# Kernel optimization log

Measured on AMD Instinct MI355X. Metric: run time of the kernel, lower is better.

## Reference

```python
import jax, jax.numpy as jnp
import numpy as np

B, S, H, E = 4, 4096, 2048, 8
TOP_K = 2

def setup_inputs() -> dict:
    key = jax.random.key(0)
    k0, k1, k2, k3, k4 = jax.random.split(key, 5)
    Hm = H // 2
    return {
        "hidden_states": jax.random.normal(k0, (B, S, H), dtype=jnp.float32),
        "W1": jax.random.normal(k1, (H, Hm), dtype=jnp.float32) * (1.0 / np.sqrt(H)),
        "b1": jnp.zeros((Hm,), dtype=jnp.float32),
        "W2": jax.random.normal(k2, (Hm, E), dtype=jnp.float32) * (1.0 / np.sqrt(Hm)),
        "b2": jnp.zeros((E,), dtype=jnp.float32),
    }

def reference(hidden_states, W1, b1, W2, b2):
    # Router MLP: Linear(H -> H//2) -> ReLU -> Dropout(eval: identity) -> Linear(H//2 -> E)
    h = jax.nn.relu(jnp.einsum("bsh,hm->bsm", hidden_states, W1) + b1)
    router_logits = jnp.einsum("bsm,me->bse", h, W2) + b2  # [B, S, E]
    probs = jax.nn.softmax(router_logits, axis=-1)
    expert_weights, expert_indices = jax.lax.top_k(probs, TOP_K)  # [B, S, 2]
    return (router_logits, expert_weights, expert_indices)
```

## Files before the change

kernel.cpp:

```cpp
#include <hip/hip_runtime.h>
#include <hip/hip_bf16.h>


#define HDIM 2048
#define HM 1024
#define NROWS 16384
#define NE 8
#define KSTEPS 64

typedef _Float16 f16;
typedef f16 f16x8 __attribute__((ext_vector_type(8)));
typedef __fp16 h16x2 __attribute__((ext_vector_type(2)));
typedef float f32x4 __attribute__((ext_vector_type(4)));

union frag8 {
  f16x8 v;
  h16x2 p[4];
};

__device__ __forceinline__ void gload16(const void* g, void* l) {
  __builtin_amdgcn_global_load_lds(
      (const __attribute__((address_space(1))) void*)g,
      (__attribute__((address_space(3))) void*)l, 16, 0, 0);
}

__global__ __launch_bounds__(256) void prep_w1(const float* __restrict__ W1,
                                               f16* __restrict__ W1s) {
  const int nb = blockIdx.x & 3;
  const int ktidx = blockIdx.x >> 2;
  const int r = threadIdx.x;
  const int n = nb * 256 + r;
  const int kt = ktidx * 32;
  f16 hi[32], lo[32];
#pragma unroll
  for (int kk = 0; kk < 32; ++kk) {
    float x = W1[(size_t)(kt + kk) * HM + n];
    f16 h = (f16)x;
    hi[kk] = h;
    lo[kk] = (f16)(x - (float)h);
  }
  f16* dst = W1s + (size_t)(nb * 64 + ktidx) * 16384 + r * 64;
#pragma unroll
  for (int sp = 0; sp < 8; ++sp) {
    int s = sp ^ (r & 7);
    f16x8 v;
#pragma unroll
    for (int j = 0; j < 8; ++j)
      v[j] = (s < 4) ? hi[8 * s + j] : lo[8 * (s - 4) + j];
    *(f16x8*)(dst + sp * 8) = v;
  }
}

__global__ __launch_bounds__(512, 2) void router_mfma(
    const float* __restrict__ X, const f16* __restrict__ W1s,
    const float* __restrict__ b1, const float* __restrict__ W2,
    float* __restrict__ pl) {
  const int bid = blockIdx.x;
  const int wg = (bid & 7) * 32 + (bid >> 3);
  const int rb = wg >> 2;
  const int nb = wg & 3;

  const int t = threadIdx.x;
  const int lane = t & 63;
  const int wave = t >> 6;
  const int wm = wave >> 2;
  const int wn = wave & 3;
  const int lane15 = lane & 15;
  const int lgrp = lane >> 4;

  extern __shared__ char smem[];

  const int srow = t >> 1;
  const int shalf = t & 1;
  const float* Xr = X + (size_t)(rb * 256 + srow) * HDIM + shalf * 16;
  const int sm = srow & 7;
  const int woff_h0 = srow * 128 + (((2 * shalf) ^ sm) << 4);
  const int woff_h1 = srow * 128 + (((2 * shalf + 1) ^ sm) << 4);
  const int woff_l0 = srow * 128 + (((4 + 2 * shalf) ^ sm) << 4);
  const int woff_l1 = srow * 128 + (((5 + 2 * shalf) ^ sm) << 4);

  const char* W1sB = (const char*)W1s + (size_t)nb * 64 * 32768;
  const int t16 = t * 16;

#define GLB(KT, BUF)                                                      \
  {                                                                       \
    char* bB_ = smem + (BUF) * 65536 + 32768;                             \
    _Pragma("unroll")                                                     \
    for (int i_ = 0; i_ < 4; ++i_)                                        \
      gload16(W1sB + (((size_t)(KT)) << 15) + i_ * 8192 + t16,            \
              bB_ + i_ * 8192 + t16);                                     \
  }

#define SPLITWR(BUF, x0, x1, x2, x3)                                      \
  {                                                                       \
    char* bA_ = smem + (BUF) * 65536;                                     \
    frag8 hi0_, hi1_, lo0_, lo1_;                                         \
    hi0_.p[0] = __builtin_amdgcn_cvt_pkrtz(x0.x, x0.y);                   \
    hi0_.p[1] = __builtin_amdgcn_cvt_pkrtz(x0.z, x0.w);                   \
    hi0_.p[2] = __builtin_amdgcn_cvt_pkrtz(x1.x, x1.y);                   \
    hi0_.p[3] = __builtin_amdgcn_cvt_pkrtz(x1.z, x1.w);                   \
    hi1_.p[0] = __builtin_amdgcn_cvt_pkrtz(x2.x, x2.y);                   \
    hi1_.p[1] = __builtin_amdgcn_cvt_pkrtz(x2.z, x2.w);                   \
    hi1_.p[2] = __builtin_amdgcn_cvt_pkrtz(x3.x, x3.y);                   \
    hi1_.p[3] = __builtin_amdgcn_cvt_pkrtz(x3.z, x3.w);                   \
    lo0_.p[0] = __builtin_amdgcn_cvt_pkrtz(x0.x - (float)hi0_.p[0][0],    \
                                           x0.y - (float)hi0_.p[0][1]);   \
    lo0_.p[1] = __builtin_amdgcn_cvt_pkrtz(x0.z - (float)hi0_.p[1][0],    \
                                           x0.w - (float)hi0_.p[1][1]);   \
    lo0_.p[2] = __builtin_amdgcn_cvt_pkrtz(x1.x - (float)hi0_.p[2][0],    \
                                           x1.y - (float)hi0_.p[2][1]);   \
    lo0_.p[3] = __builtin_amdgcn_cvt_pkrtz(x1.z - (float)hi0_.p[3][0],    \
                                           x1.w - (float)hi0_.p[3][1]);   \
    lo1_.p[0] = __builtin_amdgcn_cvt_pkrtz(x2.x - (float)hi1_.p[0][0],    \
                                           x2.y - (float)hi1_.p[0][1]);   \
    lo1_.p[1] = __builtin_amdgcn_cvt_pkrtz(x2.z - (float)hi1_.p[1][0],    \
                                           x2.w - (float)hi1_.p[1][1]);   \
    lo1_.p[2] = __builtin_amdgcn_cvt_pkrtz(x3.x - (float)hi1_.p[2][0],    \
                                           x3.y - (float)hi1_.p[2][1]);   \
    lo1_.p[3] = __builtin_amdgcn_cvt_pkrtz(x3.z - (float)hi1_.p[3][0],    \
                                           x3.w - (float)hi1_.p[3][1]);   \
    *(f16x8*)(bA_ + woff_h0) = hi0_.v;                                    \
    *(f16x8*)(bA_ + woff_h1) = hi1_.v;                                    \
    *(f16x8*)(bA_ + woff_l0) = lo0_.v;                                    \
    *(f16x8*)(bA_ + woff_l1) = lo1_.v;                                    \
  }

  f32x4 acc[8][4];
#pragma unroll
  for (int i = 0; i < 8; ++i)
#pragma unroll
    for (int j = 0; j < 4; ++j) acc[i][j] = (f32x4){0.f, 0.f, 0.f, 0.f};

  {
    GLB(0, 0);
    GLB(1, 1);
    float4 a0 = *(const float4*)(Xr + 0);
    float4 a1 = *(const float4*)(Xr + 4);
    float4 a2 = *(const float4*)(Xr + 8);
    float4 a3 = *(const float4*)(Xr + 12);
    float4 c0 = *(const float4*)(Xr + 32);
    float4 c1 = *(const float4*)(Xr + 36);
    float4 c2 = *(const float4*)(Xr + 40);
    float4 c3 = *(const float4*)(Xr + 44);
    asm volatile("s_waitcnt vmcnt(0)" ::: "memory");
    SPLITWR(0, a0, a1, a2, a3);
    SPLITWR(1, c0, c1, c2, c3);
    asm volatile("s_waitcnt lgkmcnt(0)" ::: "memory");
  }
  __builtin_amdgcn_s_barrier();

  const int arow_base = wm * 128 + lane15;
  const int offAh = ((lgrp ^ (lane15 & 7)) << 4);
  const int offAl = (((4 + lgrp) ^ (lane15 & 7)) << 4);

  int cur = 0;
#pragma unroll 1
  for (int kti = 0; kti < KSTEPS; ++kti) {
    const char* ldsA = smem + cur * 65536;
    const f16* ldsB = (const f16*)(ldsA + 32768);
    const bool stage2 = (kti + 2 < KSTEPS);

    float4 x0, x1, x2, x3;
    if (stage2) {
      const float* xs = Xr + (kti + 2) * 32;
      x0 = *(const float4*)(xs + 0);
      x1 = *(const float4*)(xs + 4);
      x2 = *(const float4*)(xs + 8);
      x3 = *(const float4*)(xs + 12);
    }

    frag8 bh[4], bl[4];
#pragma unroll
    for (int ni = 0; ni < 4; ++ni) {
      int c = wn * 64 + ni * 16 + lane15;
      bh[ni].v = *(const f16x8*)&ldsB[c * 64 + ((lgrp ^ (c & 7)) << 3)];
      bl[ni].v = *(const f16x8*)&ldsB[c * 64 + (((4 + lgrp) ^ (c & 7)) << 3)];
    }

    frag8 ah, al, nah, nal;
    {
      const char* rowp = ldsA + arow_base * 128;
      ah.v = *(const f16x8*)(rowp + offAh);
      al.v = *(const f16x8*)(rowp + offAl);
    }
#pragma unroll
    for (int mi = 0; mi < 8; ++mi) {
      if (mi < 7) {
        const char* rowp = ldsA + (arow_base + (mi + 1) * 16) * 128;
        nah.v = *(const f16x8*)(rowp + offAh);
        nal.v = *(const f16x8*)(rowp + offAl);
      }
      __builtin_amdgcn_s_setprio(1);
#pragma unroll
      for (int ni = 0; ni < 4; ++ni) {
        acc[mi][ni] = __builtin_amdgcn_mfma_f32_16x16x32_f16(
            ah.v, bh[ni].v, acc[mi][ni], 0, 0, 0);
        acc[mi][ni] = __builtin_amdgcn_mfma_f32_16x16x32_f16(
            ah.v, bl[ni].v, acc[mi][ni], 0, 0, 0);
        acc[mi][ni] = __builtin_amdgcn_mfma_f32_16x16x32_f16(
            al.v, bh[ni].v, acc[mi][ni], 0, 0, 0);
      }
      __builtin_amdgcn_s_setprio(0);
      ah = nah;
      al = nal;
    }

    if (kti == KSTEPS - 1) break;
    __builtin_amdgcn_sched_barrier(0);
    __builtin_amdgcn_s_barrier();
    if (stage2) {
      GLB(kti + 2, cur);
      asm volatile("s_waitcnt vmcnt(4)" ::: "memory");
      SPLITWR(cur, x0, x1, x2, x3);
      asm volatile("s_waitcnt lgkmcnt(0)" ::: "memory");
    } else {
      asm volatile("s_waitcnt vmcnt(0)" ::: "memory");
    }
    __builtin_amdgcn_s_barrier();
    cur ^= 1;
  }

  __syncthreads();
  float* red = (float*)smem;

  float bvals[4];
  float w2r[4][NE];
#pragma unroll
  for (int ni = 0; ni < 4; ++ni) {
    int c = nb * 256 + wn * 64 + ni * 16 + lane15;
    bvals[ni] = b1[c];
    const float* src = W2 + (size_t)c * NE;
#pragma unroll
    for (int e = 0; e < NE; ++e) w2r[ni][e] = src[e];
  }

#pragma unroll
  for (int mi = 0; mi < 8; ++mi) {
    float plr[4][NE];
#pragma unroll
    for (int j = 0; j < 4; ++j)
#pragma unroll
      for (int e = 0; e < NE; ++e) plr[j][e] = 0.f;
#pragma unroll
    for (int ni = 0; ni < 4; ++ni) {
#pragma unroll
      for (int j = 0; j < 4; ++j) {
        float h = acc[mi][ni][j] + bvals[ni];
        h = fmaxf(h, 0.f);
#pragma unroll
        for (int e = 0; e < NE; ++e) plr[j][e] = fmaf(h, w2r[ni][e], plr[j][e]);
      }
    }
#pragma unroll
    for (int m = 1; m < 16; m <<= 1)
#pragma unroll
      for (int j = 0; j < 4; ++j)
#pragma unroll
        for (int e = 0; e < NE; ++e)
          plr[j][e] += __shfl_xor(plr[j][e], m, 64);
    if (lane15 == 0) {
#pragma unroll
      for (int j = 0; j < 4; ++j) {
        int rr = wm * 128 + mi * 16 + lgrp * 4 + j;
#pragma unroll
        for (int e = 0; e < NE; ++e)
          red[(size_t)wn * 2048 + rr * NE + e] = plr[j][e];
      }
    }
  }
  __syncthreads();
  for (int i = t; i < 256 * NE; i += 512) {
    int r = i >> 3, e = i & 7;
    int row = rb * 256 + r;
    float s = red[i] + red[2048 + i] + red[4096 + i] + red[6144 + i];
    pl[((size_t)nb * NROWS + row) * NE + e] = s;
  }
}

__global__ __launch_bounds__(256) void router_finalize(
    const float* __restrict__ pl, const float* __restrict__ b2,
    float* __restrict__ out) {
  int row = blockIdx.x * 256 + threadIdx.x;
  if (row >= NROWS) return;
  float l[NE];
#pragma unroll
  for (int e = 0; e < NE; ++e) l[e] = b2[e];
  for (int nb = 0; nb < 4; ++nb) {
    const float* src = pl + ((size_t)nb * NROWS + row) * NE;
#pragma unroll
    for (int e = 0; e < NE; ++e) l[e] += src[e];
  }
#pragma unroll
  for (int e = 0; e < NE; ++e) out[(size_t)row * NE + e] = l[e];

  float m = l[0];
#pragma unroll
  for (int e = 1; e < NE; ++e) m = fmaxf(m, l[e]);
  float p[NE], s = 0.f;
#pragma unroll
  for (int e = 0; e < NE; ++e) {
    p[e] = expf(l[e] - m);
    s += p[e];
  }
  float inv = 1.f / s;

  float v0 = -1.f, v1 = -1.f;
  int i0 = 0, i1 = 0;
#pragma unroll
  for (int e = 0; e < NE; ++e) {
    float pe = p[e];
    if (pe > v0) {
      v1 = v0; i1 = i0;
      v0 = pe; i0 = e;
    } else if (pe > v1) {
      v1 = pe; i1 = e;
    }
  }
  size_t wbase = (size_t)NROWS * NE + (size_t)row * 2;
  out[wbase] = v0 * inv;
  out[wbase + 1] = v1 * inv;
  size_t ibase = (size_t)NROWS * NE + (size_t)NROWS * 2 + (size_t)row * 2;
  out[ibase] = (float)i0;
  out[ibase + 1] = (float)i1;
}

extern "C" void kernel_launch(void* const* d_in, const int* in_sizes, int n_in,
                              void* d_out, int out_size, void* d_ws,
                              size_t ws_size, hipStream_t stream) {
  const float* X = (const float*)d_in[0];
  const float* W1 = (const float*)d_in[1];
  const float* b1 = (const float*)d_in[2];
  const float* W2 = (const float*)d_in[3];
  const float* b2 = (const float*)d_in[4];
  float* out = (float*)d_out;

  float* pl = (float*)d_ws;
  f16* W1s = (f16*)((char*)d_ws + (size_t)4 * 1024 * 1024);

  (void)hipFuncSetAttribute((const void*)router_mfma,
                            hipFuncAttributeMaxDynamicSharedMemorySize, 131072);

  hipLaunchKernelGGL(prep_w1, dim3(256), dim3(256), 0, stream, W1, W1s);
  hipLaunchKernelGGL(router_mfma, dim3(256), dim3(512), 131072, stream, X, W1s,
                     b1, W2, pl);
  hipLaunchKernelGGL(router_finalize, dim3(NROWS / 256), dim3(256), 0, stream,
                     pl, b2, out);
}
```

Baseline: 206.1 us.

## Switch router GEMM from 16x16x32 to 32x32x16 MFMA tiles

Replaces the 16x16x32 f16 MFMA tiling with 32x32x16 MFMAs, each covering half the K step. The swizzled LDS fragment addressing, accumulator layout and fused ReLU/W2 epilogue are reworked to match the 32x32 output layout. The aim is to issue half as many MFMA instructions and use the larger-tile instruction, which may run more efficiently per flop. In exchange, the epilogue reduction now needs five shuffle stages over 32 lanes for 16 row groups, which adds cross-lane shuffle work.

Measured after the change: 255.9 us. 1.24x slower.

```diff
diff --git a/kernel.cpp b/kernel.cpp
--- a/kernel.cpp
+++ b/kernel.cpp
@@ -12,6 +12,7 @@
 typedef f16 f16x8 __attribute__((ext_vector_type(8)));
 typedef __fp16 h16x2 __attribute__((ext_vector_type(2)));
 typedef float f32x4 __attribute__((ext_vector_type(4)));
+typedef float f32x16 __attribute__((ext_vector_type(16)));
 
 union frag8 {
   f16x8 v;
@@ -65,8 +66,8 @@
   const int wave = t >> 6;
   const int wm = wave >> 2;
   const int wn = wave & 3;
-  const int lane15 = lane & 15;
-  const int lgrp = lane >> 4;
+  const int lane31 = lane & 31;
+  const int hi5 = lane >> 5;
 
   extern __shared__ char smem[];
 
@@ -125,11 +126,13 @@
     *(f16x8*)(bA_ + woff_l1) = lo1_.v;                                    \
   }
 
-  f32x4 acc[8][4];
-#pragma unroll
-  for (int i = 0; i < 8; ++i)
-#pragma unroll
-    for (int j = 0; j < 4; ++j) acc[i][j] = (f32x4){0.f, 0.f, 0.f, 0.f};
+  f32x16 acc[4][2];
+#pragma unroll
+  for (int i = 0; i < 4; ++i)
+#pragma unroll
+    for (int j = 0; j < 2; ++j)
+#pragma unroll
+      for (int k = 0; k < 16; ++k) acc[i][j][k] = 0.f;
 
   {
     GLB(0, 0);
@@ -149,15 +152,17 @@
   }
   __builtin_amdgcn_s_barrier();
 
-  const int arow_base = wm * 128 + lane15;
-  const int offAh = ((lgrp ^ (lane15 & 7)) << 4);
-  const int offAl = (((4 + lgrp) ^ (lane15 & 7)) << 4);
+  const int l7 = lane & 7;
+  const int offH[2] = {(((0 + hi5) ^ l7) << 4), (((2 + hi5) ^ l7) << 4)};
+  const int offL[2] = {(((4 + hi5) ^ l7) << 4), (((6 + hi5) ^ l7) << 4)};
+  const int arow0 = (wm * 128 + lane31) * 128;
+  const int bcol0 = (wn * 64 + lane31) * 128;
 
   int cur = 0;
 #pragma unroll 1
   for (int kti = 0; kti < KSTEPS; ++kti) {
     const char* ldsA = smem + cur * 65536;
-    const f16* ldsB = (const f16*)(ldsA + 32768);
+    const char* ldsB = ldsA + 32768;
     const bool stage2 = (kti + 2 < KSTEPS);
 
     float4 x0, x1, x2, x3;
@@ -169,40 +174,58 @@
       x3 = *(const float4*)(xs + 12);
     }
 
-    frag8 bh[4], bl[4];
-#pragma unroll
-    for (int ni = 0; ni < 4; ++ni) {
-      int c = wn * 64 + ni * 16 + lane15;
-      bh[ni].v = *(const f16x8*)&ldsB[c * 64 + ((lgrp ^ (c & 7)) << 3)];
-      bl[ni].v = *(const f16x8*)&ldsB[c * 64 + (((4 + lgrp) ^ (c & 7)) << 3)];
-    }
-
-    frag8 ah, al, nah, nal;
+    frag8 bh[2][2], bl[2][2];
+#pragma unroll
+    for (int ni = 0; ni < 2; ++ni) {
+      const char* cp = ldsB + bcol0 + ni * 32 * 128;
+#pragma unroll
+      for (int ks = 0; ks < 2; ++ks) {
+        bh[ni][ks].v = *(const f16x8*)(cp + offH[ks]);
+        bl[ni][ks].v = *(const f16x8*)(cp + offL[ks]);
+      }
+    }
+
+    frag8 ah[2], al[2], nah[2], nal[2];
     {
-      const char* rowp = ldsA + arow_base * 128;
-      ah.v = *(const f16x8*)(rowp + offAh);
-      al.v = *(const f16x8*)(rowp + offAl);
-    }
-#pragma unroll
-    for (int mi = 0; mi < 8; ++mi) {
-      if (mi < 7) {
-        const char* rowp = ldsA + (arow_base + (mi + 1) * 16) * 128;
-        nah.v = *(const f16x8*)(rowp + offAh);
-        nal.v = *(const f16x8*)(rowp + offAl);
+      const char* rp = ldsA + arow0;
+#pragma unroll
+      for (int ks = 0; ks < 2; ++ks) {
+        ah[ks].v = *(const f16x8*)(rp + offH[ks]);
+        al[ks].v = *(const f16x8*)(rp + offL[ks]);
+      }
+    }
+#pragma unroll
+    for (int mi = 0; mi < 4; ++mi) {
+      if (mi < 3) {
+        const char* rp = ldsA + arow0 + (mi + 1) * 32 * 128;
+#pragma unroll
+        for (int ks = 0; ks < 2; ++ks) {
+          nah[ks].v = *(const f16x8*)(rp + offH[ks]);
+          nal[ks].v = *(const f16x8*)(rp + offL[ks]);
+        }
       }
       __builtin_amdgcn_s_setprio(1);
 #pragma unroll
-      for (int ni = 0; ni < 4; ++ni) {
-        acc[mi][ni] = __builtin_amdgcn_mfma_f32_16x16x32_f16(
-            ah.v, bh[ni].v, acc[mi][ni], 0, 0, 0);
-        acc[mi][ni] = __builtin_amdgcn_mfma_f32_16x16x32_f16(
-            ah.v, bl[ni].v, acc[mi][ni], 0, 0, 0);
-        acc[mi][ni] = __builtin_amdgcn_mfma_f32_16x16x32_f16(
-            al.v, bh[ni].v, acc[mi][ni], 0, 0, 0);
+      for (int ks = 0; ks < 2; ++ks) {
+        acc[mi][0] = __builtin_amdgcn_mfma_f32_32x32x16_f16(
+            ah[ks].v, bh[0][ks].v, acc[mi][0], 0, 0, 0);
+        acc[mi][1] = __builtin_amdgcn_mfma_f32_32x32x16_f16(
+            ah[ks].v, bh[1][ks].v, acc[mi][1], 0, 0, 0);
+        acc[mi][0] = __builtin_amdgcn_mfma_f32_32x32x16_f16(
+            ah[ks].v, bl[0][ks].v, acc[mi][0], 0, 0, 0);
+        acc[mi][1] = __builtin_amdgcn_mfma_f32_32x32x16_f16(
+            ah[ks].v, bl[1][ks].v, acc[mi][1], 0, 0, 0);
+        acc[mi][0] = __builtin_amdgcn_mfma_f32_32x32x16_f16(
+            al[ks].v, bh[0][ks].v, acc[mi][0], 0, 0, 0);
+        acc[mi][1] = __builtin_amdgcn_mfma_f32_32x32x16_f16(
+            al[ks].v, bh[1][ks].v, acc[mi][1], 0, 0, 0);
       }
       __builtin_amdgcn_s_setprio(0);
-      ah = nah;
-      al = nal;
+#pragma unroll
+      for (int ks = 0; ks < 2; ++ks) {
+        ah[ks] = nah[ks];
+        al[ks] = nal[ks];
+      }
     }
 
     if (kti == KSTEPS - 1) break;
@@ -223,11 +246,11 @@
   __syncthreads();
   float* red = (float*)smem;
 
-  float bvals[4];
-  float w2r[4][NE];
-#pragma unroll
-  for (int ni = 0; ni < 4; ++ni) {
-    int c = nb * 256 + wn * 64 + ni * 16 + lane15;
+  float bvals[2];
+  float w2r[2][NE];
+#pragma unroll
+  for (int ni = 0; ni < 2; ++ni) {
+    int c = nb * 256 + wn * 64 + ni * 32 + lane31;
     bvals[ni] = b1[c];
     const float* src = W2 + (size_t)c * NE;
 #pragma unroll
@@ -235,36 +258,40 @@
   }
 
 #pragma unroll
-  for (int mi = 0; mi < 8; ++mi) {
-    float plr[4][NE];
-#pragma unroll
-    for (int j = 0; j < 4; ++j)
-#pragma unroll
-      for (int e = 0; e < NE; ++e) plr[j][e] = 0.f;
-#pragma unroll
-    for (int ni = 0; ni < 4; ++ni) {
-#pragma unroll
-      for (int j = 0; j < 4; ++j) {
-        float h = acc[mi][ni][j] + bvals[ni];
-        h = fmaxf(h, 0.f);
-#pragma unroll
-        for (int e = 0; e < NE; ++e) plr[j][e] = fmaf(h, w2r[ni][e], plr[j][e]);
-      }
-    }
-#pragma unroll
-    for (int m = 1; m < 16; m <<= 1)
+  for (int mi = 0; mi < 4; ++mi) {
+#pragma unroll
+    for (int q = 0; q < 4; ++q) {
+      float plr[4][NE];
 #pragma unroll
       for (int j = 0; j < 4; ++j)
 #pragma unroll
-        for (int e = 0; e < NE; ++e)
-          plr[j][e] += __shfl_xor(plr[j][e], m, 64);
-    if (lane15 == 0) {
-#pragma unroll
-      for (int j = 0; j < 4; ++j) {
-        int rr = wm * 128 + mi * 16 + lgrp * 4 + j;
-#pragma unroll
-        for (int e = 0; e < NE; ++e)
-          red[(size_t)wn * 2048 + rr * NE + e] = plr[j][e];
+        for (int e = 0; e < NE; ++e) plr[j][e] = 0.f;
+#pragma unroll
+      for (int ni = 0; ni < 2; ++ni) {
+#pragma unroll
+        for (int j = 0; j < 4; ++j) {
+          float h = acc[mi][ni][4 * q + j] + bvals[ni];
+          h = fmaxf(h, 0.f);
+#pragma unroll
+          for (int e = 0; e < NE; ++e)
+            plr[j][e] = fmaf(h, w2r[ni][e], plr[j][e]);
+        }
+      }
+#pragma unroll
+      for (int m = 1; m < 32; m <<= 1)
+#pragma unroll
+        for (int j = 0; j < 4; ++j)
+#pragma unroll
+          for (int e = 0; e < NE; ++e)
+            plr[j][e] += __shfl_xor(plr[j][e], m, 64);
+      if (lane31 == 0) {
+#pragma unroll
+        for (int j = 0; j < 4; ++j) {
+          int rr = wm * 128 + mi * 32 + q * 8 + hi5 * 4 + j;
+#pragma unroll
+          for (int e = 0; e < NE; ++e)
+            red[(size_t)wn * 2048 + rr * NE + e] = plr[j][e];
+        }
       }
     }
   }
```

## Use plain fp16 GEMM and recompute near-tie rows exactly in fp32

Applied to the files above, without the earlier changes.

Replaces the split-fp16 (hi/lo) three-MFMA emulation of fp32 with a single fp16 hi×hi product, halving the K-steps and cutting MFMA work by roughly two thirds. Rows whose top logits fall within a small threshold of each other are flagged via an atomic counter and recomputed exactly in fp32 by two new kernels, so top-k selection stays correct. Softmax/top-k is simplified to work on logits directly. The risk is that logits for unflagged rows carry fp16 error, and the fixed capacity on flagged rows may overflow.

Measured after the change: 541.3 us. 163% more time.

```diff
diff --git a/kernel.cpp b/kernel.cpp
--- a/kernel.cpp
+++ b/kernel.cpp
@@ -6,7 +6,8 @@
 #define HM 1024
 #define NROWS 16384
 #define NE 8
-#define KSTEPS 64
+#define KSTEPS 32
+#define TH_FLAG 0.006f
 
 typedef _Float16 f16;
 typedef f16 f16x8 __attribute__((ext_vector_type(8)));
@@ -25,34 +26,29 @@
 }
 
 __global__ __launch_bounds__(256) void prep_w1(const float* __restrict__ W1,
-                                               f16* __restrict__ W1s) {
+                                               f16* __restrict__ W1h) {
   const int nb = blockIdx.x & 3;
-  const int ktidx = blockIdx.x >> 2;
+  const int kt = blockIdx.x >> 2;
   const int r = threadIdx.x;
   const int n = nb * 256 + r;
-  const int kt = ktidx * 32;
-  f16 hi[32], lo[32];
-#pragma unroll
-  for (int kk = 0; kk < 32; ++kk) {
-    float x = W1[(size_t)(kt + kk) * HM + n];
-    f16 h = (f16)x;
-    hi[kk] = h;
-    lo[kk] = (f16)(x - (float)h);
-  }
-  f16* dst = W1s + (size_t)(nb * 64 + ktidx) * 16384 + r * 64;
+  const int k0 = kt * 64;
+  f16 hi[64];
+#pragma unroll
+  for (int kk = 0; kk < 64; ++kk)
+    hi[kk] = (f16)W1[(size_t)(k0 + kk) * HM + n];
+  f16* dst = W1h + (size_t)(nb * 32 + kt) * 16384 + r * 64;
 #pragma unroll
   for (int sp = 0; sp < 8; ++sp) {
     int s = sp ^ (r & 7);
     f16x8 v;
 #pragma unroll
-    for (int j = 0; j < 8; ++j)
-      v[j] = (s < 4) ? hi[8 * s + j] : lo[8 * (s - 4) + j];
+    for (int j = 0; j < 8; ++j) v[j] = hi[8 * s + j];
     *(f16x8*)(dst + sp * 8) = v;
   }
 }
 
 __global__ __launch_bounds__(512, 2) void router_mfma(
-    const float* __restrict__ X, const f16* __restrict__ W1s,
+    const float* __restrict__ X, const f16* __restrict__ W1h,
     const float* __restrict__ b1, const float* __restrict__ W2,
     float* __restrict__ pl) {
   const int bid = blockIdx.x;
@@ -72,14 +68,14 @@
 
   const int srow = t >> 1;
   const int shalf = t & 1;
-  const float* Xr = X + (size_t)(rb * 256 + srow) * HDIM + shalf * 16;
+  const float* Xr = X + (size_t)(rb * 256 + srow) * HDIM + shalf * 32;
   const int sm = srow & 7;
-  const int woff_h0 = srow * 128 + (((2 * shalf) ^ sm) << 4);
-  const int woff_h1 = srow * 128 + (((2 * shalf + 1) ^ sm) << 4);
-  const int woff_l0 = srow * 128 + (((4 + 2 * shalf) ^ sm) << 4);
-  const int woff_l1 = srow * 128 + (((5 + 2 * shalf) ^ sm) << 4);
-
-  const char* W1sB = (const char*)W1s + (size_t)nb * 64 * 32768;
+  int woff[4];
+#pragma unroll
+  for (int i = 0; i < 4; ++i)
+    woff[i] = srow * 128 + (((shalf * 4 + i) ^ sm) << 4);
+
+  const char* W1hB = (const char*)W1h + (size_t)nb * 32 * 32768;
   const int t16 = t * 16;
 
 #define GLB(KT, BUF)                                                      \
@@ -87,42 +83,34 @@
     char* bB_ = smem + (BUF) * 65536 + 32768;                             \
     _Pragma("unroll")                                                     \
     for (int i_ = 0; i_ < 4; ++i_)                                        \
-      gload16(W1sB + (((size_t)(KT)) << 15) + i_ * 8192 + t16,            \
+      gload16(W1hB + (((size_t)(KT)) << 15) + i_ * 8192 + t16,            \
               bB_ + i_ * 8192 + t16);                                     \
   }
 
-#define SPLITWR(BUF, x0, x1, x2, x3)                                      \
+#define HIWR(BUF, X0, X1, X2, X3, X4, X5, X6, X7)                         \
   {                                                                       \
     char* bA_ = smem + (BUF) * 65536;                                     \
-    frag8 hi0_, hi1_, lo0_, lo1_;                                         \
-    hi0_.p[0] = __builtin_amdgcn_cvt_pkrtz(x0.x, x0.y);                   \
-    hi0_.p[1] = __builtin_amdgcn_cvt_pkrtz(x0.z, x0.w);                   \
-    hi0_.p[2] = __builtin_amdgcn_cvt_pkrtz(x1.x, x1.y);                   \
-    hi0_.p[3] = __builtin_amdgcn_cvt_pkrtz(x1.z, x1.w);                   \
-    hi1_.p[0] = __builtin_amdgcn_cvt_pkrtz(x2.x, x2.y);                   \
-    hi1_.p[1] = __builtin_amdgcn_cvt_pkrtz(x2.z, x2.w);                   \
-    hi1_.p[2] = __builtin_amdgcn_cvt_pkrtz(x3.x, x3.y);                   \
-    hi1_.p[3] = __builtin_amdgcn_cvt_pkrtz(x3.z, x3.w);                   \
-    lo0_.p[0] = __builtin_amdgcn_cvt_pkrtz(x0.x - (float)hi0_.p[0][0],    \
-                                           x0.y - (float)hi0_.p[0][1]);   \
-    lo0_.p[1] = __builtin_amdgcn_cvt_pkrtz(x0.z - (float)hi0_.p[1][0],    \
-                                           x0.w - (float)hi0_.p[1][1]);   \
-    lo0_.p[2] = __builtin_amdgcn_cvt_pkrtz(x1.x - (float)hi0_.p[2][0],    \
-                                           x1.y - (float)hi0_.p[2][1]);   \
-    lo0_.p[3] = __builtin_amdgcn_cvt_pkrtz(x1.z - (float)hi0_.p[3][0],    \
-                                           x1.w - (float)hi0_.p[3][1]);   \
-    lo1_.p[0] = __builtin_amdgcn_cvt_pkrtz(x2.x - (float)hi1_.p[0][0],    \
-                                           x2.y - (float)hi1_.p[0][1]);   \
-    lo1_.p[1] = __builtin_amdgcn_cvt_pkrtz(x2.z - (float)hi1_.p[1][0],    \
-                                           x2.w - (float)hi1_.p[1][1]);   \
-    lo1_.p[2] = __builtin_amdgcn_cvt_pkrtz(x3.x - (float)hi1_.p[2][0],    \
-                                           x3.y - (float)hi1_.p[2][1]);   \
-    lo1_.p[3] = __builtin_amdgcn_cvt_pkrtz(x3.z - (float)hi1_.p[3][0],    \
-                                           x3.w - (float)hi1_.p[3][1]);   \
-    *(f16x8*)(bA_ + woff_h0) = hi0_.v;                                    \
-    *(f16x8*)(bA_ + woff_h1) = hi1_.v;                                    \
-    *(f16x8*)(bA_ + woff_l0) = lo0_.v;                                    \
-    *(f16x8*)(bA_ + woff_l1) = lo1_.v;                                    \
+    frag8 v0_, v1_, v2_, v3_;                                             \
+    v0_.p[0] = __builtin_amdgcn_cvt_pkrtz(X0.x, X0.y);                    \
+    v0_.p[1] = __builtin_amdgcn_cvt_pkrtz(X0.z, X0.w);                    \
+    v0_.p[2] = __builtin_amdgcn_cvt_pkrtz(X1.x, X1.y);                    \
+    v0_.p[3] = __builtin_amdgcn_cvt_pkrtz(X1.z, X1.w);                    \
+    v1_.p[0] = __builtin_amdgcn_cvt_pkrtz(X2.x, X2.y);                    \
+    v1_.p[1] = __builtin_amdgcn_cvt_pkrtz(X2.z, X2.w);                    \
+    v1_.p[2] = __builtin_amdgcn_cvt_pkrtz(X3.x, X3.y);                    \
+    v1_.p[3] = __builtin_amdgcn_cvt_pkrtz(X3.z, X3.w);                    \
+    v2_.p[0] = __builtin_amdgcn_cvt_pkrtz(X4.x, X4.y);                    \
+    v2_.p[1] = __builtin_amdgcn_cvt_pkrtz(X4.z, X4.w);                    \
+    v2_.p[2] = __builtin_amdgcn_cvt_pkrtz(X5.x, X5.y);                    \
+    v2_.p[3] = __builtin_amdgcn_cvt_pkrtz(X5.z, X5.w);                    \
+    v3_.p[0] = __builtin_amdgcn_cvt_pkrtz(X6.x, X6.y);                    \
+    v3_.p[1] = __builtin_amdgcn_cvt_pkrtz(X6.z, X6.w);                    \
+    v3_.p[2] = __builtin_amdgcn_cvt_pkrtz(X7.x, X7.y);                    \
+    v3_.p[3] = __builtin_amdgcn_cvt_pkrtz(X7.z, X7.w);                    \
+    *(f16x8*)(bA_ + woff[0]) = v0_.v;                                     \
+    *(f16x8*)(bA_ + woff[1]) = v1_.v;                                     \
+    *(f16x8*)(bA_ + woff[2]) = v2_.v;                                     \
+    *(f16x8*)(bA_ + woff[3]) = v3_.v;                                     \
   }
 
   f32x4 acc[8][4];
@@ -134,75 +122,71 @@
   {
     GLB(0, 0);
     GLB(1, 1);
-    float4 a0 = *(const float4*)(Xr + 0);
-    float4 a1 = *(const float4*)(Xr + 4);
-    float4 a2 = *(const float4*)(Xr + 8);
-    float4 a3 = *(const float4*)(Xr + 12);
-    float4 c0 = *(const float4*)(Xr + 32);
-    float4 c1 = *(const float4*)(Xr + 36);
-    float4 c2 = *(const float4*)(Xr + 40);
-    float4 c3 = *(const float4*)(Xr + 44);
+    float4 a[8], c[8];
+#pragma unroll
+    for (int i = 0; i < 8; ++i) a[i] = *(const float4*)(Xr + 4 * i);
+#pragma unroll
+    for (int i = 0; i < 8; ++i) c[i] = *(const float4*)(Xr + 64 + 4 * i);
     asm volatile("s_waitcnt vmcnt(0)" ::: "memory");
-    SPLITWR(0, a0, a1, a2, a3);
-    SPLITWR(1, c0, c1, c2, c3);
+    HIWR(0, a[0], a[1], a[2], a[3], a[4], a[5], a[6], a[7]);
+    HIWR(1, c[0], c[1], c[2], c[3], c[4], c[5], c[6], c[7]);
     asm volatile("s_waitcnt lgkmcnt(0)" ::: "memory");
   }
   __builtin_amdgcn_s_barrier();
 
-  const int arow_base = wm * 128 + lane15;
-  const int offAh = ((lgrp ^ (lane15 & 7)) << 4);
-  const int offAl = (((4 + lgrp) ^ (lane15 & 7)) << 4);
+  const int l7 = lane & 7;
+  const int offK0 = ((lgrp ^ l7) << 4);
+  const int offK1 = (((4 + lgrp) ^ l7) << 4);
+  const int arow0 = (wm * 128 + lane15) * 128;
+  const int bcol0 = (wn * 64 + lane15) * 128;
 
   int cur = 0;
 #pragma unroll 1
   for (int kti = 0; kti < KSTEPS; ++kti) {
     const char* ldsA = smem + cur * 65536;
-    const f16* ldsB = (const f16*)(ldsA + 32768);
+    const char* ldsB = ldsA + 32768;
     const bool stage2 = (kti + 2 < KSTEPS);
 
-    float4 x0, x1, x2, x3;
+    float4 xr[8];
     if (stage2) {
-      const float* xs = Xr + (kti + 2) * 32;
-      x0 = *(const float4*)(xs + 0);
-      x1 = *(const float4*)(xs + 4);
-      x2 = *(const float4*)(xs + 8);
-      x3 = *(const float4*)(xs + 12);
-    }
-
-    frag8 bh[4], bl[4];
+      const float* xs = Xr + (kti + 2) * 64;
+#pragma unroll
+      for (int i = 0; i < 8; ++i) xr[i] = *(const float4*)(xs + 4 * i);
+    }
+
+    frag8 b[4][2];
 #pragma unroll
     for (int ni = 0; ni < 4; ++ni) {
-      int c = wn * 64 + ni * 16 + lane15;
-      bh[ni].v = *(const f16x8*)&ldsB[c * 64 + ((lgrp ^ (c & 7)) << 3)];
-      bl[ni].v = *(const f16x8*)&ldsB[c * 64 + (((4 + lgrp) ^ (c & 7)) << 3)];
-    }
-
-    frag8 ah, al, nah, nal;
+      const char* cp = ldsB + bcol0 + ni * 16 * 128;
+      b[ni][0].v = *(const f16x8*)(cp + offK0);
+      b[ni][1].v = *(const f16x8*)(cp + offK1);
+    }
+
+    frag8 a0, a1, na0, na1;
     {
-      const char* rowp = ldsA + arow_base * 128;
-      ah.v = *(const f16x8*)(rowp + offAh);
-      al.v = *(const f16x8*)(rowp + offAl);
+      const char* rp = ldsA + arow0;
+      a0.v = *(const f16x8*)(rp + offK0);
+      a1.v = *(const f16x8*)(rp + offK1);
     }
 #pragma unroll
     for (int mi = 0; mi < 8; ++mi) {
       if (mi < 7) {
-        const char* rowp = ldsA + (arow_base + (mi + 1) * 16) * 128;
-        nah.v = *(const f16x8*)(rowp + offAh);
-        nal.v = *(const f16x8*)(rowp + offAl);
+        const char* rp = ldsA + arow0 + (mi + 1) * 16 * 128;
+        na0.v = *(const f16x8*)(rp + offK0);
+        na1.v = *(const f16x8*)(rp + offK1);
       }
       __builtin_amdgcn_s_setprio(1);
 #pragma unroll
-      for (int ni = 0; ni < 4; ++ni) {
+      for (int ni = 0; ni < 4; ++ni)
         acc[mi][ni] = __builtin_amdgcn_mfma_f32_16x16x32_f16(
-            ah.v, bh[ni].v, acc[mi][ni], 0, 0, 0);
+            a0.v, b[ni][0].v, acc[mi][ni], 0, 0, 0);
+#pragma unroll
+      for (int ni = 0; ni < 4; ++ni)
         acc[mi][ni] = __builtin_amdgcn_mfma_f32_16x16x32_f16(
-            ah.v, bl[ni].v, acc[mi][ni], 0, 0, 0);
-        acc[mi][ni] = __builtin_amdgcn_mfma_f32_16x16x32_f16(
-            al.v, bh[ni].v, acc[mi][ni], 0, 0, 0);
-      }
+            a1.v, b[ni][1].v, acc[mi][ni], 0, 0, 0);
       __builtin_amdgcn_s_setprio(0);
-      ah = nah;
-      al = nal;
+      a0 = na0;
+      a1 = na1;
     }
 
     if (kti == KSTEPS - 1) break;
@@ -211,7 +195,7 @@
     if (stage2) {
       GLB(kti + 2, cur);
       asm volatile("s_waitcnt vmcnt(4)" ::: "memory");
-      SPLITWR(cur, x0, x1, x2, x3);
+      HIWR(cur, xr[0], xr[1], xr[2], xr[3], xr[4], xr[5], xr[6], xr[7]);
       asm volatile("s_waitcnt lgkmcnt(0)" ::: "memory");
     } else {
       asm volatile("s_waitcnt vmcnt(0)" ::: "memory");
@@ -279,7 +263,7 @@
 
 __global__ __launch_bounds__(256) void router_finalize(
     const float* __restrict__ pl, const float* __restrict__ b2,
-    float* __restrict__ out) {
+    float* __restrict__ out, int* __restrict__ meta, int cap) {
   int row = blockIdx.x * 256 + threadIdx.x;
   if (row >= NROWS) return;
   float l[NE];
@@ -293,35 +277,127 @@
 #pragma unroll
   for (int e = 0; e < NE; ++e) out[(size_t)row * NE + e] = l[e];
 
-  float m = l[0];
-#pragma unroll
-  for (int e = 1; e < NE; ++e) m = fmaxf(m, l[e]);
-  float p[NE], s = 0.f;
+  float v0 = -1e30f, v1 = -1e30f, v2 = -1e30f;
+  int i0 = 0, i1 = 0;
 #pragma unroll
   for (int e = 0; e < NE; ++e) {
-    p[e] = expf(l[e] - m);
-    s += p[e];
-  }
+    float le = l[e];
+    if (le > v0) {
+      v2 = v1; v1 = v0; i1 = i0; v0 = le; i0 = e;
+    } else if (le > v1) {
+      v2 = v1; v1 = le; i1 = e;
+    } else if (le > v2) {
+      v2 = le;
+    }
+  }
+  float s = 0.f;
+#pragma unroll
+  for (int e = 0; e < NE; ++e) s += expf(l[e] - v0);
   float inv = 1.f / s;
 
-  float v0 = -1.f, v1 = -1.f;
-  int i0 = 0, i1 = 0;
-#pragma unroll
-  for (int e = 0; e < NE; ++e) {
-    float pe = p[e];
-    if (pe > v0) {
-      v1 = v0; i1 = i0;
-      v0 = pe; i0 = e;
-    } else if (pe > v1) {
-      v1 = pe; i1 = e;
-    }
-  }
   size_t wbase = (size_t)NROWS * NE + (size_t)row * 2;
-  out[wbase] = v0 * inv;
-  out[wbase + 1] = v1 * inv;
+  out[wbase] = inv;
+  out[wbase + 1] = expf(v1 - v0) * inv;
   size_t ibase = (size_t)NROWS * NE + (size_t)NROWS * 2 + (size_t)row * 2;
   out[ibase] = (float)i0;
   out[ibase + 1] = (float)i1;
+
+  if ((v0 - v1 < TH_FLAG) || (v1 - v2 < TH_FLAG)) {
+    int p = atomicAdd(meta, 1);
+    if (p < cap) meta[4 + p] = row;
+  }
+}
+
+__global__ __launch_bounds__(256) void recompute(
+    const float* __restrict__ X, const float* __restrict__ W1,
+    const int* __restrict__ meta, float* __restrict__ hpart, int cap) {
+  __shared__ float w1s[1024][9];
+  const int cc = blockIdx.x & 127;
+  const int ks = blockIdx.x >> 7;
+  const int t = threadIdx.x;
+  const int k0 = ks * 1024, c0 = cc * 8;
+  for (int i = t; i < 8192; i += 256) {
+    int k = i >> 3, c = i & 7;
+    w1s[k][c] = W1[(size_t)(k0 + k) * HM + c0 + c];
+  }
+  __syncthreads();
+  const int n = min(meta[0], cap);
+  const int j = t >> 5;
+  const int kk = t & 31;
+  for (int p = 0; p < n; ++p) {
+    int row = meta[4 + p];
+    const float* xr = X + (size_t)row * HDIM + k0;
+    float acc = 0.f;
+#pragma unroll
+    for (int i = 0; i < 32; ++i)
+      acc = fmaf(xr[kk + 32 * i], w1s[kk + 32 * i][j], acc);
+#pragma unroll
+    for (int m = 1; m < 32; m <<= 1) acc += __shfl_xor(acc, m, 64);
+    if (kk == 0) hpart[((size_t)ks * cap + p) * 1024 + c0 + j] = acc;
+  }
+}
+
+__global__ __launch_bounds__(256) void fin2(
+    const float* __restrict__ b1, const float* __restrict__ W2,
+    const float* __restrict__ b2, const int* __restrict__ meta,
+    const float* __restrict__ hpart, float* __restrict__ out, int cap) {
+  const int b = blockIdx.x;
+  const int n = min(meta[0], cap);
+  if (b >= n) return;
+  const int row = meta[4 + b];
+  const int t = threadIdx.x;
+  float plr[NE];
+#pragma unroll
+  for (int e = 0; e < NE; ++e) plr[e] = 0.f;
+#pragma unroll
+  for (int q = 0; q < 4; ++q) {
+    int c = t + q * 256;
+    float h = hpart[(size_t)b * 1024 + c] +
+              hpart[((size_t)cap + b) * 1024 + c] + b1[c];
+    h = fmaxf(h, 0.f);
+#pragma unroll
+    for (int e = 0; e < NE; ++e)
+      plr[e] = fmaf(h, W2[(size_t)c * NE + e], plr[e]);
+  }
+#pragma unroll
+  for (int m = 1; m < 64; m <<= 1)
+#pragma unroll
+    for (int e = 0; e < NE; ++e) plr[e] += __shfl_xor(plr[e], m, 64);
+  __shared__ float red[4][NE];
+  if ((t & 63) == 0) {
+#pragma unroll
+    for (int e = 0; e < NE; ++e) red[t >> 6][e] = plr[e];
+  }
+  __syncthreads();
+  if (t == 0) {
+    float l[NE];
+#pragma unroll
+    for (int e = 0; e < NE; ++e)
+      l[e] = red[0][e] + red[1][e] + red[2][e] + red[3][e] + b2[e];
+#pragma unroll
+    for (int e = 0; e < NE; ++e) out[(size_t)row * NE + e] = l[e];
+    float v0 = -1e30f, v1 = -1e30f;
+    int i0 = 0, i1 = 0;
+#pragma unroll
+    for (int e = 0; e < NE; ++e) {
+      float le = l[e];
+      if (le > v0) {
+        v1 = v0; i1 = i0; v0 = le; i0 = e;
+      } else if (le > v1) {
+        v1 = le; i1 = e;
+      }
+    }
+    float s = 0.f;
+#pragma unroll
+    for (int e = 0; e < NE; ++e) s += expf(l[e] - v0);
+    float inv = 1.f / s;
+    size_t wbase = (size_t)NROWS * NE + (size_t)row * 2;
+    out[wbase] = inv;
+    out[wbase + 1] = expf(v1 - v0) * inv;
+    size_t ibase = (size_t)NROWS * NE + (size_t)NROWS * 2 + (size_t)row * 2;
+    out[ibase] = (float)i0;
+    out[ibase + 1] = (float)i1;
+  }
 }
 
 extern "C" void kernel_launch(void* const* d_in, const int* in_sizes, int n_in,
@@ -334,15 +410,28 @@
   const float* b2 = (const float*)d_in[4];
   float* out = (float*)d_out;
 
+  const size_t META_OFF = (size_t)6 * 1024 * 1024;
+  const size_t HPART_OFF = META_OFF + 512 * 1024;
   float* pl = (float*)d_ws;
-  f16* W1s = (f16*)((char*)d_ws + (size_t)4 * 1024 * 1024);
+  f16* W1h = (f16*)((char*)d_ws + (size_t)2 * 1024 * 1024);
+  int* meta = (int*)((char*)d_ws + META_OFF);
+  float* hpart = (float*)((char*)d_ws + HPART_OFF);
+  int cap = 0;
+  if (ws_size > HPART_OFF + 8192)
+    cap = (int)((ws_size - HPART_OFF) / 8192);
+  if (cap > 768) cap = 768;
 
   (void)hipFuncSetAttribute((const void*)router_mfma,
                             hipFuncAttributeMaxDynamicSharedMemorySize, 131072);
 
-  hipLaunchKernelGGL(prep_w1, dim3(256), dim3(256), 0, stream, W1, W1s);
-  hipLaunchKernelGGL(router_mfma, dim3(256), dim3(512), 131072, stream, X, W1s,
+  hipLaunchKernelGGL(prep_w1, dim3(128), dim3(256), 0, stream, W1, W1h);
+  (void)hipMemsetAsync(meta, 0, 4, stream);
+  hipLaunchKernelGGL(router_mfma, dim3(256), dim3(512), 131072, stream, X, W1h,
                      b1, W2, pl);
   hipLaunchKernelGGL(router_finalize, dim3(NROWS / 256), dim3(256), 0, stream,
-                     pl, b2, out);
-}
+                     pl, b2, out, meta, cap);
+  hipLaunchKernelGGL(recompute, dim3(256), dim3(256), 0, stream, X, W1, meta,
+                     hpart, cap);
+  hipLaunchKernelGGL(fin2, dim3(cap > 0 ? cap : 1), dim3(256), 0, stream, b1,
+                     W2, b2, meta, hpart, out, cap);
+}
```
